# Kernel optimization log

Measured on AMD Instinct MI355X. Metric: run time of the kernel, lower is better.

Reference implementation:

```python
import jax, jax.numpy as jnp
import numpy as np

N = 512          # nsites (even)
B = 1024         # batch of spin configurations
HALF = N // 2

# static off-diagonal scatter indices (~eye mask)
_ROWS, _COLS = np.nonzero(~np.eye(N, dtype=bool))


def setup_inputs() -> dict:
    key = jax.random.key(0)
    k_f, k_x = jax.random.split(key)
    scale = np.float32(np.sqrt(2.0 * np.e / N))
    F = jax.random.normal(k_f, (N * N - N,), jnp.float32) * scale
    # balanced +/-1 spins per sample (zero magnetization), random permutation per row
    base = jnp.concatenate([jnp.ones(HALF, jnp.float32), -jnp.ones(HALF, jnp.float32)])
    keys = jax.random.split(k_x, B)
    x = jax.vmap(lambda k: jax.random.permutation(k, base))(keys)
    return {"x": x, "F": F}


def reference(x, F):
    # scatter parameters into dense off-diagonal pair matrix (shared across batch)
    F_full = jnp.zeros((N, N), F.dtype).at[_ROWS, _COLS].set(F)

    def single(xs):
        # spin system: up occupation then down occupation -> exactly N particles
        occ = jnp.concatenate([xs > 0, xs <= 0])
        idx = jnp.flatnonzero(occ, size=N)          # [N] int
        up = idx[:HALF]                              # up-site indices in [0, N)
        dn = idx[HALF:] - N                          # down-site indices in [0, N)
        sub = F_full[up[:, None], dn[None, :]]       # [N/2, N/2] gathered submatrix
        return jnp.linalg.det(sub)

    return jax.vmap(single)(x)  # [B]
```

## Files before the change

kernel.cpp:

```cpp
#include <hip/hip_runtime.h>

#define NN 512
#define NM1 511
#define PCT(r, j) pcT[(r) * 13 + (j)]

#define T16(X, K) X(K,0) X(K,1) X(K,2) X(K,3) X(K,4) X(K,5) X(K,6) X(K,7) \
  X(K,8) X(K,9) X(K,10) X(K,11) X(K,12) X(K,13) X(K,14) X(K,15)
#define T4x16(X) T16(X,0) T16(X,1) T16(X,2) T16(X,3)
#define T16S(X) X(0) X(1) X(2) X(3) X(4) X(5) X(6) X(7) \
  X(8) X(9) X(10) X(11) X(12) X(13) X(14) X(15)
#define P8(X, K) X(K,0) X(K,1) X(K,2) X(K,3) X(K,4) X(K,5) X(K,6) X(K,7)
#define P4x8(X) P8(X,0) P8(X,1) P8(X,2) P8(X,3)

__device__ __forceinline__ float rdlane(float v, int l) {
  return __uint_as_float(
      (unsigned)__builtin_amdgcn_readlane((int)__float_as_uint(v), l));
}

__global__ __attribute__((amdgpu_waves_per_eu(4, 4))) __launch_bounds__(1024)
void det_lu_kernel(
    const float* __restrict__ x,
    const float* __restrict__ F,
    float* __restrict__ out) {
  __shared__ __align__(16) float pcT[256 * 13];
  __shared__ __align__(16) float lbuf[8 * 256];
  __shared__ __align__(16) float Ubuf[8 * 260];
  __shared__ float livef[256];
  __shared__ int   perm[256];
  __shared__ int   upbuf[256];
  __shared__ int   dnbuf[256];
  __shared__ int   wavecnt[8];
  __shared__ int   totinv;
  __shared__ float ldspad[12100];

  const int tid = threadIdx.x;
  const int L   = tid & 63;
  const int w   = tid >> 6;

  const float* xrow = x + (size_t)blockIdx.x * NN;

  if ((int)blockIdx.x < 0) ((volatile float*)ldspad)[tid] = 1.0f;

  bool pos = false;
  unsigned long long mask = 0;
  if (tid < NN) {
    float xv = xrow[tid];
    pos = xv > 0.0f;
    mask = __ballot(pos);
    if (L == 0) wavecnt[w] = __popcll(mask);
  }
  if (tid == 0) totinv = 0;
  if (tid < 256) livef[tid] = 1.0f;
  __syncthreads();
  if (tid < NN) {
    int base = 0;
    for (int i = 0; i < w; i++) base += wavecnt[i];
    int pbelow = __popcll(mask & ((1ull << L) - 1ull));
    if (pos) upbuf[base + pbelow] = tid;
    else     dnbuf[(64 * w - base) + (L - pbelow)] = tid;
  }
  __syncthreads();

#define DECLC(M) const int cg##M = dnbuf[16 * w + (M)];
  T16S(DECLC)
  const int rg0 = upbuf[L];
  const int rg1 = upbuf[L + 64];
  const int rg2 = upbuf[L + 128];
  const int rg3 = upbuf[L + 192];
#define DECLA(K, M)                                                         \
  float a##K##_##M = (cg##M == rg##K)                                       \
      ? 0.0f                                                                \
      : F[(size_t)rg##K * NM1 + cg##M - (cg##M > rg##K ? 1 : 0)];
  T4x16(DECLA)

  if (w == 0) {
#define S0(K, M) if ((M) < 8) PCT(L + 64 * (K), (M)) = a##K##_##M;
    T4x16(S0)
  }
  double det = 1.0;
  __syncthreads();

#define DPPMAX(CTRL) {                                                      \
    unsigned _t = (unsigned)__builtin_amdgcn_update_dpp(                    \
        0, (int)key, (CTRL), 0xf, 0xf, false);                              \
    key = key > _t ? key : _t; }
#define BCJ(K, J, S) if ((J) >= (S)) uv##J = rdlane(pr##K##_##J, lp);
#define BCARM(K, S)                                                         \
    if (kp == (K)) { BCJ(K,0,S) BCJ(K,1,S) BCJ(K,2,S) BCJ(K,3,S)            \
                     BCJ(K,4,S) BCJ(K,5,S) BCJ(K,6,S) BCJ(K,7,S) }
#define LSTEP(K, S)                                                         \
    float l##K = ((dead4 >> (K)) & 1u) ? 0.0f : pr##K##_##S * invp;         \
    pr##K##_##S = l##K;
#define UPD(K, J, S)                                                        \
    if ((J) > (S)) pr##K##_##J = fmaf(-l##K, uv##J, pr##K##_##J);
#define UPDJ(J, S) UPD(0,J,S) UPD(1,J,S) UPD(2,J,S) UPD(3,J,S)
#define STQ(K, Q, M0, M1, M2, M3)                                           \
    if (kp == (K)) *reinterpret_cast<float4*>(&Ubuf[sb + 4 * (Q)]) =        \
        make_float4(a##K##_##M0, a##K##_##M1, a##K##_##M2, a##K##_##M3);
#define STHK(K)                                                             \
    STQ(K,0,0,1,2,3) STQ(K,1,4,5,6,7)                                       \
    STQ(K,2,8,9,10,11) STQ(K,3,12,13,14,15)
#define FSTEP(S) {                                                          \
    unsigned b0 = (dead4 & 1u) ? 0u                                         \
        : ((__float_as_uint(fabsf(pr0_##S)) & 0xFFFFFF00u) | (unsigned)L);  \
    unsigned b1 = (dead4 & 2u) ? 0u                                         \
        : ((__float_as_uint(fabsf(pr1_##S)) & 0xFFFFFF00u) | (unsigned)(L + 64)); \
    unsigned b2 = (dead4 & 4u) ? 0u                                         \
        : ((__float_as_uint(fabsf(pr2_##S)) & 0xFFFFFF00u) | (unsigned)(L + 128)); \
    unsigned b3 = (dead4 & 8u) ? 0u                                         \
        : ((__float_as_uint(fabsf(pr3_##S)) & 0xFFFFFF00u) | (unsigned)(L + 192)); \
    unsigned m01 = b0 > b1 ? b0 : b1, m23 = b2 > b3 ? b2 : b3;              \
    unsigned key = m01 > m23 ? m01 : m23;                                   \
    DPPMAX(0x111) DPPMAX(0x112) DPPMAX(0x114) DPPMAX(0x118)                 \
    DPPMAX(0x142) DPPMAX(0x143)                                             \
    const int pv = __builtin_amdgcn_readlane((int)key, 63) & 255;           \
    const int kp = pv >> 6, lp = pv & 63;                                   \
    if (lp == L) dead4 |= 1u << kp;                                         \
    float uv0 = 0.f, uv1 = 0.f, uv2 = 0.f, uv3 = 0.f;                       \
    float uv4 = 0.f, uv5 = 0.f, uv6 = 0.f, uv7 = 0.f;                       \
    BCARM(0,S) BCARM(1,S) BCARM(2,S) BCARM(3,S)                             \
    const float piv = uv##S;                                                \
    det *= (double)piv;                                                     \
    const float invp = 1.0f / piv;                                          \
    LSTEP(0,S) LSTEP(1,S) LSTEP(2,S) LSTEP(3,S)                             \
    UPDJ(0,S) UPDJ(1,S) UPDJ(2,S) UPDJ(3,S)                                 \
    UPDJ(4,S) UPDJ(5,S) UPDJ(6,S) UPDJ(7,S)                                 \
    if (w == 0) {                                                           \
      lbuf[(S) * 256 + L      ] = l0;                                       \
      lbuf[(S) * 256 + L +  64] = l1;                                       \
      lbuf[(S) * 256 + L + 128] = l2;                                       \
      lbuf[(S) * 256 + L + 192] = l3;                                       \
      if (L == lp) livef[pv] = 0.0f;                                        \
      if (L == 0) perm[P * 8 + (S)] = pv;                                   \
    }                                                                       \
    if (trailing && L == lp) {                                              \
      const int sb = (S) * 260 + 16 * w;                                    \
      STHK(0) STHK(1) STHK(2) STHK(3)                                       \
    }                                                                       \
  }

#define TUROW(K, A, B, C, D)                                                \
    a##K##_##A = fmaf(-lk##K, uq.x, a##K##_##A);                            \
    a##K##_##B = fmaf(-lk##K, uq.y, a##K##_##B);                            \
    a##K##_##C = fmaf(-lk##K, uq.z, a##K##_##C);                            \
    a##K##_##D = fmaf(-lk##K, uq.w, a##K##_##D);
#define TUQ(A, B, C, D)                                                     \
    TUROW(0, A, B, C, D) TUROW(1, A, B, C, D)                               \
    TUROW(2, A, B, C, D) TUROW(3, A, B, C, D)

#pragma unroll 1
  for (int P = 0; P < 32; P++) {
    const bool trailing  = (2 * w + 1 > P);
    const bool factoring = trailing || (w == 0);

    if (factoring) {
#define LDP(K, J) float pr##K##_##J = PCT(L + 64 * (K), (J));
      P4x8(LDP)
      unsigned dead4 = 0u;
      FSTEP(0) FSTEP(1) FSTEP(2) FSTEP(3)
      FSTEP(4) FSTEP(5) FSTEP(6) FSTEP(7)
    }
    __syncthreads();

    if (tid < 256) {
      const int j = tid;
      float u[8];
#pragma unroll
      for (int t = 0; t < 8; t++) {
        int pt = perm[P * 8 + t];
        float acc = Ubuf[t * 260 + j];
#pragma unroll
        for (int s2 = 0; s2 < t; s2++) acc = fmaf(-lbuf[s2 * 256 + pt], u[s2], acc);
        u[t] = acc;
        Ubuf[t * 260 + j] = acc;
      }
    }
    __syncthreads();

    if (trailing) {
#pragma unroll 1
      for (int t = 0; t < 8; t++) {
        const int lb = t * 256 + L;
        const float lk0 = lbuf[lb];
        const float lk1 = lbuf[lb + 64];
        const float lk2 = lbuf[lb + 128];
        const float lk3 = lbuf[lb + 192];
        const float* ub = &Ubuf[t * 260 + 16 * w];
        { const float4 uq = *reinterpret_cast<const float4*>(ub + 0);
          TUQ(0, 1, 2, 3) }
        { const float4 uq = *reinterpret_cast<const float4*>(ub + 4);
          TUQ(4, 5, 6, 7) }
        { const float4 uq = *reinterpret_cast<const float4*>(ub + 8);
          TUQ(8, 9, 10, 11) }
        { const float4 uq = *reinterpret_cast<const float4*>(ub + 12);
          TUQ(12, 13, 14, 15) }
      }
    }
    {
      const int wstar = (P + 1) >> 1, h = (P + 1) & 1;
      if (P < 31 && w == wstar) {
        const float lv0 = livef[L];
        const float lv1 = livef[L + 64];
        const float lv2 = livef[L + 128];
        const float lv3 = livef[L + 192];
#define SEa(K, M) if ((M) < 8)  PCT(L + 64*(K), (M))     = a##K##_##M * lv##K;
#define SEb(K, M) if ((M) >= 8) PCT(L + 64*(K), (M) - 8) = a##K##_##M * lv##K;
        if (h == 0) { T4x16(SEa) }
        else        { T4x16(SEb) }
      }
    }
    __syncthreads();
  }

  int myinv = 0;
  {
    const int i0 = tid & 255;
    const int cbase = (tid >> 8) * 64;
    const int pi = perm[i0];
#pragma unroll 8
    for (int j = 0; j < 64; j++) {
      int jj = cbase + j;
      if (jj > i0 && perm[jj] < pi) myinv++;
    }
  }
#pragma unroll
  for (int off = 32; off; off >>= 1) myinv += __shfl_xor(myinv, off);
  if (L == 0) atomicAdd(&totinv, myinv);
  __syncthreads();
  if (tid == 0) out[blockIdx.x] = (float)((totinv & 1) ? -det : det);
}

extern "C" void kernel_launch(void* const* d_in, const int* in_sizes, int n_in,
                              void* d_out, int out_size, void* d_ws, size_t ws_size,
                              hipStream_t stream) {
  const float* x = (const float*)d_in[0];
  const float* F = (const float*)d_in[1];
  float* out = (float*)d_out;
  const int B = out_size;
  hipLaunchKernelGGL(det_lu_kernel, dim3(B), dim3(1024), 0, stream, x, F, out);
}
```

Measured before the change: 977.4 us.

## Interleave column ownership across waves to balance trailing LU update work

```diff
diff --git a/kernel.cpp b/kernel.cpp
--- a/kernel.cpp
+++ b/kernel.cpp
@@ -61,7 +61,7 @@
   }
   __syncthreads();
 
-#define DECLC(M) const int cg##M = dnbuf[16 * w + (M)];
+#define DECLC(M) const int cg##M = dnbuf[4 * w + 64 * ((M) >> 2) + ((M) & 3)];
   T16S(DECLC)
   const int rg0 = upbuf[L];
   const int rg1 = upbuf[L + 64];
@@ -73,10 +73,21 @@
       : F[(size_t)rg##K * NM1 + cg##M - (cg##M > rg##K ? 1 : 0)];
   T4x16(DECLA)
 
-  if (w == 0) {
-#define S0(K, M) if ((M) < 8) PCT(L + 64 * (K), (M)) = a##K##_##M;
-    T4x16(S0)
-  }
+#define SD4(K, M0, M1, M2, M3, OFF, LV)                                     \
+    PCT(L + 64 * (K), (OFF) + 0) = a##K##_##M0 * (LV);                      \
+    PCT(L + 64 * (K), (OFF) + 1) = a##K##_##M1 * (LV);                      \
+    PCT(L + 64 * (K), (OFF) + 2) = a##K##_##M2 * (LV);                      \
+    PCT(L + 64 * (K), (OFF) + 3) = a##K##_##M3 * (LV);
+#define SEEDM(M0, M1, M2, M3, OFF) {                                        \
+    const float lv0 = livef[L];                                             \
+    const float lv1 = livef[L + 64];                                        \
+    const float lv2 = livef[L + 128];                                       \
+    const float lv3 = livef[L + 192];                                       \
+    SD4(0, M0, M1, M2, M3, OFF, lv0) SD4(1, M0, M1, M2, M3, OFF, lv1)       \
+    SD4(2, M0, M1, M2, M3, OFF, lv2) SD4(3, M0, M1, M2, M3, OFF, lv3) }
+
+  if (w == 0) SEEDM(0, 1, 2, 3, 0)
+  if (w == 1) SEEDM(0, 1, 2, 3, 4)
   double det = 1.0;
   __syncthreads();
 
@@ -94,12 +105,12 @@
 #define UPD(K, J, S)                                                        \
     if ((J) > (S)) pr##K##_##J = fmaf(-l##K, uv##J, pr##K##_##J);
 #define UPDJ(J, S) UPD(0,J,S) UPD(1,J,S) UPD(2,J,S) UPD(3,J,S)
-#define STQ(K, Q, M0, M1, M2, M3)                                           \
-    if (kp == (K)) *reinterpret_cast<float4*>(&Ubuf[sb + 4 * (Q)]) =        \
+#define STQm(K, M0, M1, M2, M3, MOFF)                                       \
+    if (kp == (K)) *reinterpret_cast<float4*>(&Ubuf[sb + (MOFF)]) =         \
         make_float4(a##K##_##M0, a##K##_##M1, a##K##_##M2, a##K##_##M3);
 #define STHK(K)                                                             \
-    STQ(K,0,0,1,2,3) STQ(K,1,4,5,6,7)                                       \
-    STQ(K,2,8,9,10,11) STQ(K,3,12,13,14,15)
+    STQm(K, 0, 1, 2, 3, 0)     STQm(K, 4, 5, 6, 7, 64)                      \
+    STQm(K, 8, 9, 10, 11, 128) STQm(K, 12, 13, 14, 15, 192)
 #define FSTEP(S) {                                                          \
     unsigned b0 = (dead4 & 1u) ? 0u                                         \
         : ((__float_as_uint(fabsf(pr0_##S)) & 0xFFFFFF00u) | (unsigned)L);  \
@@ -133,29 +144,47 @@
       if (L == lp) livef[pv] = 0.0f;                                        \
       if (L == 0) perm[P * 8 + (S)] = pv;                                   \
     }                                                                       \
-    if (trailing && L == lp) {                                              \
-      const int sb = (S) * 260 + 16 * w;                                    \
+    if (L == lp) {                                                          \
+      const int sb = (S) * 260 + 4 * w;                                     \
       STHK(0) STHK(1) STHK(2) STHK(3)                                       \
     }                                                                       \
   }
 
-#define TUROW(K, A, B, C, D)                                                \
-    a##K##_##A = fmaf(-lk##K, uq.x, a##K##_##A);                            \
-    a##K##_##B = fmaf(-lk##K, uq.y, a##K##_##B);                            \
-    a##K##_##C = fmaf(-lk##K, uq.z, a##K##_##C);                            \
-    a##K##_##D = fmaf(-lk##K, uq.w, a##K##_##D);
-#define TUQ(A, B, C, D)                                                     \
-    TUROW(0, A, B, C, D) TUROW(1, A, B, C, D)                               \
-    TUROW(2, A, B, C, D) TUROW(3, A, B, C, D)
+#define TUQm(T, M0, M1, M2, M3, MOFF) {                                     \
+    const float4 uq = *reinterpret_cast<const float4*>(                     \
+        &Ubuf[(T) * 260 + 4 * w + (MOFF)]);                                 \
+    a0_##M0 = fmaf(-pr0_##T, uq.x, a0_##M0);                                \
+    a0_##M1 = fmaf(-pr0_##T, uq.y, a0_##M1);                                \
+    a0_##M2 = fmaf(-pr0_##T, uq.z, a0_##M2);                                \
+    a0_##M3 = fmaf(-pr0_##T, uq.w, a0_##M3);                                \
+    a1_##M0 = fmaf(-pr1_##T, uq.x, a1_##M0);                                \
+    a1_##M1 = fmaf(-pr1_##T, uq.y, a1_##M1);                                \
+    a1_##M2 = fmaf(-pr1_##T, uq.z, a1_##M2);                                \
+    a1_##M3 = fmaf(-pr1_##T, uq.w, a1_##M3);                                \
+    a2_##M0 = fmaf(-pr2_##T, uq.x, a2_##M0);                                \
+    a2_##M1 = fmaf(-pr2_##T, uq.y, a2_##M1);                                \
+    a2_##M2 = fmaf(-pr2_##T, uq.z, a2_##M2);                                \
+    a2_##M3 = fmaf(-pr2_##T, uq.w, a2_##M3);                                \
+    a3_##M0 = fmaf(-pr3_##T, uq.x, a3_##M0);                                \
+    a3_##M1 = fmaf(-pr3_##T, uq.y, a3_##M1);                                \
+    a3_##M2 = fmaf(-pr3_##T, uq.z, a3_##M2);                                \
+    a3_##M3 = fmaf(-pr3_##T, uq.w, a3_##M3); }
+#define TUTT(T)                                                             \
+    if (lv0q) TUQm(T, 0, 1, 2, 3, 0)                                        \
+    if (lv1q) TUQm(T, 4, 5, 6, 7, 64)                                       \
+    if (lv2q) TUQm(T, 8, 9, 10, 11, 128)                                    \
+    if (lv3q) TUQm(T, 12, 13, 14, 15, 192)
 
 #pragma unroll 1
   for (int P = 0; P < 32; P++) {
-    const bool trailing  = (2 * w + 1 > P);
-    const bool factoring = trailing || (w == 0);
+    const int  thr = 2 * (P + 1);
+    const bool factoring = (w + 48 >= thr) || (w == 0);
+#define DPR(K, J) float pr##K##_##J;
+    P4x8(DPR)
 
     if (factoring) {
-#define LDP(K, J) float pr##K##_##J = PCT(L + 64 * (K), (J));
-      P4x8(LDP)
+#define LDPA(K, J) pr##K##_##J = PCT(L + 64 * (K), (J));
+      P4x8(LDPA)
       unsigned dead4 = 0u;
       FSTEP(0) FSTEP(1) FSTEP(2) FSTEP(3)
       FSTEP(4) FSTEP(5) FSTEP(6) FSTEP(7)
@@ -177,36 +206,30 @@
     }
     __syncthreads();
 
-    if (trailing) {
-#pragma unroll 1
-      for (int t = 0; t < 8; t++) {
-        const int lb = t * 256 + L;
-        const float lk0 = lbuf[lb];
-        const float lk1 = lbuf[lb + 64];
-        const float lk2 = lbuf[lb + 128];
-        const float lk3 = lbuf[lb + 192];
-        const float* ub = &Ubuf[t * 260 + 16 * w];
-        { const float4 uq = *reinterpret_cast<const float4*>(ub + 0);
-          TUQ(0, 1, 2, 3) }
-        { const float4 uq = *reinterpret_cast<const float4*>(ub + 4);
-          TUQ(4, 5, 6, 7) }
-        { const float4 uq = *reinterpret_cast<const float4*>(ub + 8);
-          TUQ(8, 9, 10, 11) }
-        { const float4 uq = *reinterpret_cast<const float4*>(ub + 12);
-          TUQ(12, 13, 14, 15) }
+    {
+      const bool lv0q = (w      >= thr);
+      const bool lv1q = (w + 16 >= thr);
+      const bool lv2q = (w + 32 >= thr);
+      const bool lv3q = (w + 48 >= thr);
+      TUTT(0) TUTT(1) TUTT(2) TUTT(3)
+      TUTT(4) TUTT(5) TUTT(6) TUTT(7)
+    }
+
+    if (P < 31) {
+      const int qa = 2 * (P + 1);
+      if (w == (qa & 15)) {
+        const int ma = qa >> 4;
+        if      (ma == 0) SEEDM(0, 1, 2, 3, 0)
+        else if (ma == 1) SEEDM(4, 5, 6, 7, 0)
+        else if (ma == 2) SEEDM(8, 9, 10, 11, 0)
+        else              SEEDM(12, 13, 14, 15, 0)
       }
-    }
-    {
-      const int wstar = (P + 1) >> 1, h = (P + 1) & 1;
-      if (P < 31 && w == wstar) {
-        const float lv0 = livef[L];
-        const float lv1 = livef[L + 64];
-        const float lv2 = livef[L + 128];
-        const float lv3 = livef[L + 192];
-#define SEa(K, M) if ((M) < 8)  PCT(L + 64*(K), (M))     = a##K##_##M * lv##K;
-#define SEb(K, M) if ((M) >= 8) PCT(L + 64*(K), (M) - 8) = a##K##_##M * lv##K;
-        if (h == 0) { T4x16(SEa) }
-        else        { T4x16(SEb) }
+      if (w == ((qa + 1) & 15)) {
+        const int mb = (qa + 1) >> 4;
+        if      (mb == 0) SEEDM(0, 1, 2, 3, 4)
+        else if (mb == 1) SEEDM(4, 5, 6, 7, 4)
+        else if (mb == 2) SEEDM(8, 9, 10, 11, 4)
+        else              SEEDM(12, 13, 14, 15, 4)
       }
     }
     __syncthreads();
```

New measurement: 1.058 ms. 1.08x slower.

## Factor panel in one wave and fold triangular solve into trailing update

Applied to the files above, without the earlier changes.

```diff
diff --git a/kernel.cpp b/kernel.cpp
--- a/kernel.cpp
+++ b/kernel.cpp
@@ -15,6 +15,11 @@
 __device__ __forceinline__ float rdlane(float v, int l) {
   return __uint_as_float(
       (unsigned)__builtin_amdgcn_readlane((int)__float_as_uint(v), l));
+}
+__device__ __forceinline__ float fastrcp(float v) {
+  float r;
+  asm("v_rcp_f32 %0, %1" : "=v"(r) : "v"(v));
+  return r;
 }
 
 __global__ __attribute__((amdgpu_waves_per_eu(4, 4))) __launch_bounds__(1024)
@@ -94,12 +99,6 @@
 #define UPD(K, J, S)                                                        \
     if ((J) > (S)) pr##K##_##J = fmaf(-l##K, uv##J, pr##K##_##J);
 #define UPDJ(J, S) UPD(0,J,S) UPD(1,J,S) UPD(2,J,S) UPD(3,J,S)
-#define STQ(K, Q, M0, M1, M2, M3)                                           \
-    if (kp == (K)) *reinterpret_cast<float4*>(&Ubuf[sb + 4 * (Q)]) =        \
-        make_float4(a##K##_##M0, a##K##_##M1, a##K##_##M2, a##K##_##M3);
-#define STHK(K)                                                             \
-    STQ(K,0,0,1,2,3) STQ(K,1,4,5,6,7)                                       \
-    STQ(K,2,8,9,10,11) STQ(K,3,12,13,14,15)
 #define FSTEP(S) {                                                          \
     unsigned b0 = (dead4 & 1u) ? 0u                                         \
         : ((__float_as_uint(fabsf(pr0_##S)) & 0xFFFFFF00u) | (unsigned)L);  \
@@ -121,39 +120,71 @@
     BCARM(0,S) BCARM(1,S) BCARM(2,S) BCARM(3,S)                             \
     const float piv = uv##S;                                                \
     det *= (double)piv;                                                     \
-    const float invp = 1.0f / piv;                                          \
+    const float invp = fastrcp(piv);                                        \
     LSTEP(0,S) LSTEP(1,S) LSTEP(2,S) LSTEP(3,S)                             \
     UPDJ(0,S) UPDJ(1,S) UPDJ(2,S) UPDJ(3,S)                                 \
     UPDJ(4,S) UPDJ(5,S) UPDJ(6,S) UPDJ(7,S)                                 \
-    if (w == 0) {                                                           \
-      lbuf[(S) * 256 + L      ] = l0;                                       \
-      lbuf[(S) * 256 + L +  64] = l1;                                       \
-      lbuf[(S) * 256 + L + 128] = l2;                                       \
-      lbuf[(S) * 256 + L + 192] = l3;                                       \
-      if (L == lp) livef[pv] = 0.0f;                                        \
-      if (L == 0) perm[P * 8 + (S)] = pv;                                   \
-    }                                                                       \
-    if (trailing && L == lp) {                                              \
-      const int sb = (S) * 260 + 16 * w;                                    \
-      STHK(0) STHK(1) STHK(2) STHK(3)                                       \
-    }                                                                       \
-  }
-
-#define TUROW(K, A, B, C, D)                                                \
-    a##K##_##A = fmaf(-lk##K, uq.x, a##K##_##A);                            \
-    a##K##_##B = fmaf(-lk##K, uq.y, a##K##_##B);                            \
-    a##K##_##C = fmaf(-lk##K, uq.z, a##K##_##C);                            \
-    a##K##_##D = fmaf(-lk##K, uq.w, a##K##_##D);
-#define TUQ(A, B, C, D)                                                     \
-    TUROW(0, A, B, C, D) TUROW(1, A, B, C, D)                               \
-    TUROW(2, A, B, C, D) TUROW(3, A, B, C, D)
+    lbuf[(S) * 256 + L      ] = l0;                                         \
+    lbuf[(S) * 256 + L +  64] = l1;                                         \
+    lbuf[(S) * 256 + L + 128] = l2;                                         \
+    lbuf[(S) * 256 + L + 192] = l3;                                         \
+    if (L == lp) livef[pv] = 0.0f;                                          \
+    if (L == 0) perm[P * 8 + (S)] = pv;                                     \
+  }
+
+#define STQW(T, K)                                                          \
+    if (L == (p##T & 63)) {                                                 \
+      const int ub = (T) * 260 + 16 * w;                                    \
+      *reinterpret_cast<float4*>(&Ubuf[ub + 0]) =                           \
+          make_float4(a##K##_0, a##K##_1, a##K##_2, a##K##_3);              \
+      *reinterpret_cast<float4*>(&Ubuf[ub + 4]) =                           \
+          make_float4(a##K##_4, a##K##_5, a##K##_6, a##K##_7);              \
+      *reinterpret_cast<float4*>(&Ubuf[ub + 8]) =                           \
+          make_float4(a##K##_8, a##K##_9, a##K##_10, a##K##_11);            \
+      *reinterpret_cast<float4*>(&Ubuf[ub + 12]) =                          \
+          make_float4(a##K##_12, a##K##_13, a##K##_14, a##K##_15);          \
+    }
+#define STASHT(T) {                                                         \
+    const int kpt = p##T >> 6;                                              \
+    if (kpt == 0)      { STQW(T, 0) }                                       \
+    else if (kpt == 1) { STQW(T, 1) }                                       \
+    else if (kpt == 2) { STQW(T, 2) }                                       \
+    else               { STQW(T, 3) }                                       \
+  }
+#define LDG(K, T) float g##K##_##T = lbuf[(T) * 256 + L + 64 * (K)];
+#define GSTEP(S, T) {                                                       \
+    const float c = lbuf[(S) * 256 + p##T];                                 \
+    g0_##S = fmaf(-g0_##T, c, g0_##S);                                      \
+    g1_##S = fmaf(-g1_##T, c, g1_##S);                                      \
+    g2_##S = fmaf(-g2_##T, c, g2_##S);                                      \
+    g3_##S = fmaf(-g3_##T, c, g3_##S); }
+#define TUQ2(T, Q, A_, B_, C_, D_) {                                        \
+    const float4 uq = *reinterpret_cast<const float4*>(                     \
+        &Ubuf[(T) * 260 + 16 * w + 4 * (Q)]);                               \
+    a0_##A_ = fmaf(-g0_##T, uq.x, a0_##A_);                                 \
+    a0_##B_ = fmaf(-g0_##T, uq.y, a0_##B_);                                 \
+    a0_##C_ = fmaf(-g0_##T, uq.z, a0_##C_);                                 \
+    a0_##D_ = fmaf(-g0_##T, uq.w, a0_##D_);                                 \
+    a1_##A_ = fmaf(-g1_##T, uq.x, a1_##A_);                                 \
+    a1_##B_ = fmaf(-g1_##T, uq.y, a1_##B_);                                 \
+    a1_##C_ = fmaf(-g1_##T, uq.z, a1_##C_);                                 \
+    a1_##D_ = fmaf(-g1_##T, uq.w, a1_##D_);                                 \
+    a2_##A_ = fmaf(-g2_##T, uq.x, a2_##A_);                                 \
+    a2_##B_ = fmaf(-g2_##T, uq.y, a2_##B_);                                 \
+    a2_##C_ = fmaf(-g2_##T, uq.z, a2_##C_);                                 \
+    a2_##D_ = fmaf(-g2_##T, uq.w, a2_##D_);                                 \
+    a3_##A_ = fmaf(-g3_##T, uq.x, a3_##A_);                                 \
+    a3_##B_ = fmaf(-g3_##T, uq.y, a3_##B_);                                 \
+    a3_##C_ = fmaf(-g3_##T, uq.z, a3_##C_);                                 \
+    a3_##D_ = fmaf(-g3_##T, uq.w, a3_##D_); }
+#define TUTT(T) TUQ2(T, 0, 0, 1, 2, 3) TUQ2(T, 1, 4, 5, 6, 7)               \
+                TUQ2(T, 2, 8, 9, 10, 11) TUQ2(T, 3, 12, 13, 14, 15)
 
 #pragma unroll 1
   for (int P = 0; P < 32; P++) {
-    const bool trailing  = (2 * w + 1 > P);
-    const bool factoring = trailing || (w == 0);
-
-    if (factoring) {
+    const bool trailing = (2 * w + 1 > P);
+
+    if (w == 0) {
 #define LDP(K, J) float pr##K##_##J = PCT(L + 64 * (K), (J));
       P4x8(LDP)
       unsigned dead4 = 0u;
@@ -162,40 +193,26 @@
     }
     __syncthreads();
 
-    if (tid < 256) {
-      const int j = tid;
-      float u[8];
-#pragma unroll
-      for (int t = 0; t < 8; t++) {
-        int pt = perm[P * 8 + t];
-        float acc = Ubuf[t * 260 + j];
-#pragma unroll
-        for (int s2 = 0; s2 < t; s2++) acc = fmaf(-lbuf[s2 * 256 + pt], u[s2], acc);
-        u[t] = acc;
-        Ubuf[t * 260 + j] = acc;
-      }
-    }
-    __syncthreads();
-
     if (trailing) {
-#pragma unroll 1
-      for (int t = 0; t < 8; t++) {
-        const int lb = t * 256 + L;
-        const float lk0 = lbuf[lb];
-        const float lk1 = lbuf[lb + 64];
-        const float lk2 = lbuf[lb + 128];
-        const float lk3 = lbuf[lb + 192];
-        const float* ub = &Ubuf[t * 260 + 16 * w];
-        { const float4 uq = *reinterpret_cast<const float4*>(ub + 0);
-          TUQ(0, 1, 2, 3) }
-        { const float4 uq = *reinterpret_cast<const float4*>(ub + 4);
-          TUQ(4, 5, 6, 7) }
-        { const float4 uq = *reinterpret_cast<const float4*>(ub + 8);
-          TUQ(8, 9, 10, 11) }
-        { const float4 uq = *reinterpret_cast<const float4*>(ub + 12);
-          TUQ(12, 13, 14, 15) }
-      }
-    }
+      const int p0 = perm[P * 8 + 0], p1 = perm[P * 8 + 1];
+      const int p2 = perm[P * 8 + 2], p3 = perm[P * 8 + 3];
+      const int p4 = perm[P * 8 + 4], p5 = perm[P * 8 + 5];
+      const int p6 = perm[P * 8 + 6], p7 = perm[P * 8 + 7];
+      STASHT(0) STASHT(1) STASHT(2) STASHT(3)
+      STASHT(4) STASHT(5) STASHT(6) STASHT(7)
+      asm volatile("s_waitcnt lgkmcnt(0)" ::: "memory");
+      P4x8(LDG)
+      GSTEP(6,7)
+      GSTEP(5,7) GSTEP(5,6)
+      GSTEP(4,7) GSTEP(4,6) GSTEP(4,5)
+      GSTEP(3,7) GSTEP(3,6) GSTEP(3,5) GSTEP(3,4)
+      GSTEP(2,7) GSTEP(2,6) GSTEP(2,5) GSTEP(2,4) GSTEP(2,3)
+      GSTEP(1,7) GSTEP(1,6) GSTEP(1,5) GSTEP(1,4) GSTEP(1,3) GSTEP(1,2)
+      GSTEP(0,7) GSTEP(0,6) GSTEP(0,5) GSTEP(0,4) GSTEP(0,3) GSTEP(0,2) GSTEP(0,1)
+      TUTT(0) TUTT(1) TUTT(2) TUTT(3)
+      TUTT(4) TUTT(5) TUTT(6) TUTT(7)
+    }
+
     {
       const int wstar = (P + 1) >> 1, h = (P + 1) & 1;
       if (P < 31 && w == wstar) {
```

Measured after the change: 1.706 ms. 1.75x slower.
